# Performance work log

Hardware: AMD Instinct MI355X
Metric: run time of the kernel (lower is better)

The kernel has to match this reference:

```python
import math
import jax, jax.numpy as jnp
import numpy as np

B, D, H, W, K = 32, 256, 64, 64, 6
CTX = 256
TEMP = 0.5
EPS_LN = 1e-5


def _layernorm(x, g, b):
    mu = x.mean(-1, keepdims=True)
    var = ((x - mu) ** 2).mean(-1, keepdims=True)
    return (x - mu) * jax.lax.rsqrt(var + EPS_LN) * g + b


def _linear(x, w, b):
    return x @ w.T + b


def _gru_cell(x, h, wih, bih, whh, bhh):
    gi = x @ wih.T + bih
    gh = h @ whh.T + bhh
    i_r, i_z, i_n = jnp.split(gi, 3, axis=-1)
    h_r, h_z, h_n = jnp.split(gh, 3, axis=-1)
    r = jax.nn.sigmoid(i_r + h_r)
    z = jax.nn.sigmoid(i_z + h_z)
    n = jnp.tanh(i_n + r * h_n)
    return (1.0 - z) * n + z * h


def setup_inputs() -> dict:
    key = jax.random.key(0)
    ks = jax.random.split(key, 24)
    s = 0.05
    p = {
        'features': jax.random.normal(ks[0], (B, D, H, W), jnp.float32),
        'task_context': jax.random.normal(ks[1], (B, CTX), jnp.float32),
        'ctx_w1': jax.random.normal(ks[2], (D, CTX), jnp.float32) * s,
        'ctx_b1': jnp.zeros((D,), jnp.float32),
        'ctx_w2': jax.random.normal(ks[3], (K * D, D), jnp.float32) * s,
        'ctx_b2': jnp.zeros((K * D,), jnp.float32),
        'q_w': jax.random.normal(ks[4], (D, D), jnp.float32) * s,
        'q_b': jnp.zeros((D,), jnp.float32),
        'k_w': jax.random.normal(ks[5], (D, D), jnp.float32) * s,
        'k_b': jnp.zeros((D,), jnp.float32),
        'v_w': jax.random.normal(ks[6], (D, D), jnp.float32) * s,
        'v_b': jnp.zeros((D,), jnp.float32),
        'qn_g': jnp.ones((D,), jnp.float32),
        'qn_b': jnp.zeros((D,), jnp.float32),
        'fn_g': jnp.ones((D,), jnp.float32),
        'fn_b': jnp.zeros((D,), jnp.float32),
        'stop_w1': jax.random.normal(ks[7], (D // 2, D + 1), jnp.float32) * s,
        'stop_b1': jnp.zeros((D // 2,), jnp.float32),
        'stop_w2': jax.random.normal(ks[8], (1, D // 2), jnp.float32) * s,
        'stop_b2': jnp.zeros((1,), jnp.float32),
        'gru_wih': jax.random.normal(ks[9], (3 * D, D), jnp.float32) * s,
        'gru_bih': jnp.zeros((3 * D,), jnp.float32),
        'gru_whh': jax.random.normal(ks[10], (3 * D, D), jnp.float32) * s,
        'gru_bhh': jnp.zeros((3 * D,), jnp.float32),
    }
    return p


def _forward(features, task_context, ctx_w1, ctx_b1, ctx_w2, ctx_b2,
             q_w, q_b, k_w, k_b, v_w, v_b, qn_g, qn_b, fn_g, fn_b,
             stop_w1, stop_b1, stop_w2, stop_b2,
             gru_wih, gru_bih, gru_whh, gru_bhh):
    scale = math.sqrt(D)
    N = H * W
    # task-conditioned clue queries: (B, K, D), clamped
    h1 = jax.nn.gelu(_linear(task_context, ctx_w1, ctx_b1), approximate=False)
    clue_queries = _linear(h1, ctx_w2, ctx_b2).reshape(B, K, D)
    clue_queries = jnp.clip(clue_queries, -10.0, 10.0)

    # (B, N, D), normalized; k/v projections are loop-invariant -> hoist
    feats = jnp.transpose(features, (0, 2, 3, 1)).reshape(B, N, D)
    feats = _layernorm(feats, fn_g, fn_b)
    kp = _linear(feats, k_w, k_b)  # (B, N, D)
    vp = _linear(feats, v_w, v_b)  # (B, N, D)

    rows = jnp.repeat(jnp.arange(H, dtype=jnp.float32), W)  # (N,)
    cols = jnp.tile(jnp.arange(W, dtype=jnp.float32), H)    # (N,)
    max_entropy = math.log(N + 1e-6)

    def step(carry, qk):
        query_state, cum_mask = carry  # (B,D), (B,N)
        query = _layernorm(qk + query_state, qn_g, qn_b)
        q = _linear(query, q_w, q_b)  # (B, D)
        scores = jnp.einsum('bd,bnd->bn', q, kp) / scale
        scores = scores + jnp.log(jnp.clip(cum_mask, 1e-6))
        scores = jnp.clip(scores, -50.0, 50.0)
        logits = jnp.clip(scores / max(TEMP, 1e-10), -50.0, 50.0)
        attn = jnp.clip(jax.nn.softmax(logits, axis=-1), 1e-8)  # (B, N)
        row_c = attn @ rows
        col_c = attn @ cols
        centroid = jnp.stack([row_c, col_c], axis=-1)  # (B, 2)
        attended = jnp.einsum('bn,bnd->bd', attn, vp)  # (B, D)
        new_state = _gru_cell(attended, query_state, gru_wih, gru_bih, gru_whh, gru_bhh)
        a = jnp.clip(attn, 1e-6)
        entropy = -(a * jnp.log(a)).sum(-1, keepdims=True) / max_entropy
        s1 = jax.nn.gelu(_linear(jnp.concatenate([attended, entropy], -1), stop_w1, stop_b1), approximate=False)
        stop_raw = _linear(s1, stop_w2, stop_b2)[:, 0]
        stop = 4.0 * jnp.tanh(stop_raw / 4.0)
        new_mask = jnp.clip(cum_mask * (1.0 - 0.9 * jax.lax.stop_gradient(attn)), 1e-6)
        return (new_state, new_mask), (centroid, attn.reshape(B, H, W), stop)

    init = (jnp.zeros((B, D), jnp.float32), jnp.ones((B, N), jnp.float32))
    qks = jnp.transpose(clue_queries, (1, 0, 2))  # (K, B, D)
    _, (cents, attns, stops) = jax.lax.scan(step, init, qks)
    centroids = jnp.transpose(cents, (1, 0, 2))        # (B, K, 2)
    attention_maps = jnp.transpose(attns, (1, 0, 2, 3))  # (B, K, H, W)
    stop_logits = jnp.transpose(stops, (1, 0))          # (B, K)
    return centroids, attention_maps, stop_logits


def reference(features, task_context, ctx_w1, ctx_b1, ctx_w2, ctx_b2,
              q_w, q_b, k_w, k_b, v_w, v_b, qn_g, qn_b, fn_g, fn_b,
              stop_w1, stop_b1, stop_w2, stop_b2,
              gru_wih, gru_bih, gru_whh, gru_bhh):
    return _forward(features, task_context, ctx_w1, ctx_b1, ctx_w2, ctx_b2,
                    q_w, q_b, k_w, k_b, v_w, v_b, qn_g, qn_b, fn_g, fn_b,
                    stop_w1, stop_b1, stop_w2, stop_b2,
                    gru_wih, gru_bih, gru_whh, gru_bhh)
```

## Files before the change

### kernel.cpp

```cpp
#include <hip/hip_runtime.h>
#include <hip/hip_bf16.h>

#define NB 32
#define ND 256
#define NN_ 4096
#define NK 6

typedef short bf16x8 __attribute__((ext_vector_type(8)));
typedef float f32x4 __attribute__((ext_vector_type(4)));

__device__ __forceinline__ float bf2f(unsigned int u) {
    union { unsigned int i; float f; } v; v.i = (u & 0xffffu) << 16; return v.f;
}
__device__ __forceinline__ unsigned short f2bf(float f) {
    __hip_bfloat16 h = __float2bfloat16(f);
    return *reinterpret_cast<unsigned short*>(&h);
}
__device__ __forceinline__ float gelu_exact(float x) {
    return 0.5f * x * (1.0f + erff(x * 0.70710678118654752f));
}

__global__ void k_setup(const float* __restrict__ kw, const float* __restrict__ vw,
                        unsigned short* __restrict__ kwb, unsigned short* __restrict__ vwb,
                        float* __restrict__ mask, float* __restrict__ accs,
                        float* __restrict__ sumev0,
                        const float* __restrict__ tc, const float* __restrict__ w1,
                        const float* __restrict__ b1, const float* __restrict__ w2,
                        const float* __restrict__ b2, float* __restrict__ clue) {
    __shared__ __align__(16) float tcs[256];
    __shared__ __align__(16) float h1[256];
    int blk = blockIdx.x, t = threadIdx.x;
    if (blk < 1059) {
        int i = blk * 256 + t;
        if (i < 65536) kwb[i] = f2bf(kw[i]);
        else if (i < 131072) vwb[i - 65536] = f2bf(vw[i - 65536]);
        else if (i < 262144) mask[i - 131072] = 1.f;
        else if (i < 262912) accs[i - 262144] = 0.f;
        else if (i < 271104) sumev0[i - 262912] = 0.f;
        return;
    }
    int b = blk - 1059;
    tcs[t] = tc[b * 256 + t];
    __syncthreads();
    const float4* wr = (const float4*)(w1 + (size_t)t * 256);
    const float4* xs = (const float4*)tcs;
    float acc = b1[t];
#pragma unroll 8
    for (int i = 0; i < 64; ++i) {
        float4 w = wr[i], x = xs[i];
        acc += w.x * x.x + w.y * x.y + w.z * x.z + w.w * x.w;
    }
    h1[t] = gelu_exact(acc);
    __syncthreads();
    const float4* hs = (const float4*)h1;
    for (int r = 0; r < 6; ++r) {
        int row = r * 256 + t;
        const float4* w2r = (const float4*)(w2 + (size_t)row * 256);
        float a2 = b2[row];
#pragma unroll 8
        for (int i = 0; i < 64; ++i) {
            float4 w = w2r[i], x = hs[i];
            a2 += w.x * x.x + w.y * x.y + w.z * x.z + w.w * x.w;
        }
        clue[b * 1536 + row] = fminf(fmaxf(a2, -10.f), 10.f);
    }
}

__global__ __launch_bounds__(256, 2) void k_kv(
    const float* __restrict__ features, const float* __restrict__ fn_g,
    const float* __restrict__ fn_b, const unsigned short* __restrict__ kwb,
    const unsigned short* __restrict__ vwb, const float* __restrict__ kb,
    const float* __restrict__ vb, unsigned short* __restrict__ kp,
    unsigned short* __restrict__ vp) {
    int tile = blockIdx.x, b = blockIdx.y;
    int n0 = tile * 128;
    int t = threadIdx.x;

    __shared__ __align__(16) unsigned short A[32768];
    unsigned int* A32 = reinterpret_cast<unsigned int*>(A);

    int dd = t & 15, nq = t >> 4;
#pragma unroll
    for (int hh = 0; hh < 2; ++hh) {
        const float* fb = features + (size_t)b * 1048576 + n0 + hh * 64 + nq * 4;
        unsigned int pk[8][4];
        float s[4] = {0, 0, 0, 0}, s2[4] = {0, 0, 0, 0};
#pragma unroll
        for (int p = 0; p < 8; ++p) {
            int d0 = p * 32 + dd * 2;
            float4 a0 = *reinterpret_cast<const float4*>(fb + (size_t)d0 * 4096);
            float4 a1 = *reinterpret_cast<const float4*>(fb + (size_t)(d0 + 1) * 4096);
            s[0] += a0.x + a1.x; s2[0] += a0.x * a0.x + a1.x * a1.x;
            s[1] += a0.y + a1.y; s2[1] += a0.y * a0.y + a1.y * a1.y;
            s[2] += a0.z + a1.z; s2[2] += a0.z * a0.z + a1.z * a1.z;
            s[3] += a0.w + a1.w; s2[3] += a0.w * a0.w + a1.w * a1.w;
            pk[p][0] = (unsigned int)f2bf(a0.x) | ((unsigned int)f2bf(a1.x) << 16);
            pk[p][1] = (unsigned int)f2bf(a0.y) | ((unsigned int)f2bf(a1.y) << 16);
            pk[p][2] = (unsigned int)f2bf(a0.z) | ((unsigned int)f2bf(a1.z) << 16);
            pk[p][3] = (unsigned int)f2bf(a0.w) | ((unsigned int)f2bf(a1.w) << 16);
        }
#pragma unroll
        for (int m = 1; m < 16; m <<= 1) {
#pragma unroll
            for (int k = 0; k < 4; ++k) {
                s[k] += __shfl_xor(s[k], m, 64);
                s2[k] += __shfl_xor(s2[k], m, 64);
            }
        }
        float mm[4], rr[4];
#pragma unroll
        for (int k = 0; k < 4; ++k) {
            float mean = s[k] * (1.f / 256.f);
            float var = s2[k] * (1.f / 256.f) - mean * mean;
            mm[k] = mean; rr[k] = rsqrtf(var + 1e-5f);
        }
        int qdw = dd >> 2, jw = dd & 3;
#pragma unroll
        for (int p = 0; p < 8; ++p) {
            int d0 = p * 32 + dd * 2;
            float g0 = fn_g[d0], g1 = fn_g[d0 + 1];
            float e0 = fn_b[d0], e1 = fn_b[d0 + 1];
#pragma unroll
            for (int k = 0; k < 4; ++k) {
                int ln = hh * 64 + nq * 4 + k;
                int nt = ln >> 4, r = ln & 15;
                float x0 = bf2f(pk[p][k]);
                float x1 = bf2f(pk[p][k] >> 16);
                unsigned int lo = f2bf((x0 - mm[k]) * rr[k] * g0 + e0);
                unsigned int hi = f2bf((x1 - mm[k]) * rr[k] * g1 + e1);
                A32[((nt * 8 + p) * 64 + qdw * 16 + r) * 4 + jw] = lo | (hi << 16);
            }
        }
    }
    __syncthreads();

    int lane = t & 63, wv = t >> 6;
    int r = lane & 15, qd = lane >> 4;
#pragma unroll
    for (int ntt = 0; ntt < 2; ++ntt) {
        bf16x8 bfrag[4][8];
#pragma unroll
        for (int q4 = 0; q4 < 4; ++q4)
#pragma unroll
            for (int ks = 0; ks < 8; ++ks)
                bfrag[q4][ks] = *reinterpret_cast<const bf16x8*>(
                    &A[(((ntt * 4 + q4) * 8 + ks) * 64 + lane) * 8]);
#pragma unroll
        for (int mat = 0; mat < 2; ++mat) {
            const unsigned short* wb = mat ? vwb : kwb;
            const float* bias = mat ? vb : kb;
            unsigned short* outp = mat ? vp : kp;
#pragma unroll
            for (int dtl = 0; dtl < 4; ++dtl) {
                int dt = wv * 4 + dtl;
                const unsigned short* wrow = wb + (size_t)(dt * 16 + r) * 256 + qd * 8;
                f32x4 acc0 = {0, 0, 0, 0}, acc1 = {0, 0, 0, 0};
                f32x4 acc2 = {0, 0, 0, 0}, acc3 = {0, 0, 0, 0};
#pragma unroll
                for (int ks = 0; ks < 8; ++ks) {
                    bf16x8 af = *reinterpret_cast<const bf16x8*>(wrow + ks * 32);
                    acc0 = __builtin_amdgcn_mfma_f32_16x16x32_bf16(af, bfrag[0][ks], acc0, 0, 0, 0);
                    acc1 = __builtin_amdgcn_mfma_f32_16x16x32_bf16(af, bfrag[1][ks], acc1, 0, 0, 0);
                    acc2 = __builtin_amdgcn_mfma_f32_16x16x32_bf16(af, bfrag[2][ks], acc2, 0, 0, 0);
                    acc3 = __builtin_amdgcn_mfma_f32_16x16x32_bf16(af, bfrag[3][ks], acc3, 0, 0, 0);
                }
                int dbase = dt * 16 + qd * 4;
                float b0_ = bias[dbase], b1_ = bias[dbase + 1];
                float b2_ = bias[dbase + 2], b3_ = bias[dbase + 3];
                f32x4 aa[4] = {acc0, acc1, acc2, acc3};
#pragma unroll
                for (int q4 = 0; q4 < 4; ++q4) {
                    int n_g = n0 + (ntt * 4 + q4) * 16 + r;
                    unsigned int lo = ((unsigned int)f2bf(aa[q4][1] + b1_) << 16)
                                    | (unsigned int)f2bf(aa[q4][0] + b0_);
                    unsigned int hi = ((unsigned int)f2bf(aa[q4][3] + b3_) << 16)
                                    | (unsigned int)f2bf(aa[q4][2] + b2_);
                    *reinterpret_cast<uint2*>(outp + ((size_t)(b * 4096 + n_g)) * 256 + dbase)
                        = make_uint2(lo, hi);
                }
            }
        }
    }
}

__global__ __launch_bounds__(256, 4) void k_qscore(
    const float* __restrict__ clue, const float* __restrict__ gacc,
    const float* __restrict__ state_prev, float* __restrict__ state_cur,
    const float* __restrict__ qn_g, const float* __restrict__ qn_b,
    const float* __restrict__ q_w, const float* __restrict__ q_b,
    const unsigned short* __restrict__ kp, const unsigned short* __restrict__ vp,
    const float* __restrict__ mask, float* __restrict__ escore,
    float* __restrict__ accs, float* __restrict__ sumev,
    const float* __restrict__ sumev_prev,
    const float* __restrict__ sw1, const float* __restrict__ sb1,
    const float* __restrict__ sw2, const float* __restrict__ sb2,
    float* __restrict__ out_cent, float* __restrict__ out_stop, int kstep) {
    int c = blockIdx.x, b = blockIdx.y, t = threadIdx.x;
    int lane = t & 63, wv = t >> 6;
    __shared__ __align__(16) float qs[256];
    __shared__ float ash[256];
    __shared__ __align__(16) float part[8][264];
    __shared__ float sred[8];
    if (c == 16) {
        if (kstep == 0) return;
        int kp_ = kstep - 1;
        float inv = 1.f / accs[kp_ * 128 + b];
        qs[t] = sumev_prev[b * 256 + t] * inv;
        __syncthreads();
        float entv = -accs[kp_ * 128 + 96 + b] * 0.12022458674074826f;
        float v = 0.f;
        if (t < 128) {
            const float* wr = sw1 + (size_t)t * 257;
            float acc = sb1[t];
#pragma unroll 8
            for (int i = 0; i < 256; ++i) acc += qs[i] * wr[i];
            acc += entv * wr[256];
            v = gelu_exact(acc) * sw2[t];
        }
#pragma unroll
        for (int off = 32; off > 0; off >>= 1) v += __shfl_down(v, off, 64);
        if (lane == 0) sred[wv] = v;
        __syncthreads();
        if (t == 0) {
            float sraw = sb2[0] + sred[0] + sred[1] + sred[2] + sred[3];
            out_stop[b * 6 + kp_] = 4.f * tanhf(sraw * 0.25f);
            out_cent[(b * 6 + kp_) * 2 + 0] = accs[kp_ * 128 + 32 + b];
            out_cent[(b * 6 + kp_) * 2 + 1] = accs[kp_ * 128 + 64 + b];
        }
        return;
    }
    float h = 0.f;
    if (kstep > 0) {
        float sr = gacc[(b * 4 + 0) * 256 + t];
        float sz = gacc[(b * 4 + 1) * 256 + t];
        float gin = gacc[(b * 4 + 2) * 256 + t];
        float ghn = gacc[(b * 4 + 3) * 256 + t];
        float r = 1.f / (1.f + expf(-sr));
        float z = 1.f / (1.f + expf(-sz));
        float nv = tanhf(gin + r * ghn);
        h = (1.f - z) * nv + z * state_prev[b * 256 + t];
    }
    if (c == 0) state_cur[b * 256 + t] = h;
    float x = clue[(b * 6 + kstep) * 256 + t] + h;
    float s = x, s2 = x * x;
#pragma unroll
    for (int off = 32; off > 0; off >>= 1) {
        s += __shfl_down(s, off, 64);
        s2 += __shfl_down(s2, off, 64);
    }
    if (lane == 0) { sred[wv] = s; sred[4 + wv] = s2; }
    __syncthreads();
    float muv = (sred[0] + sred[1] + sred[2] + sred[3]) * (1.f / 256.f);
    float var = (sred[4] + sred[5] + sred[6] + sred[7]) * (1.f / 256.f) - muv * muv;
    float rs = rsqrtf(var + 1e-5f);
    qs[t] = (x - muv) * rs * qn_g[t] + qn_b[t];
    __syncthreads();
    const float4* wr = (const float4*)(q_w + (size_t)t * 256);
    const float4* xs4 = (const float4*)qs;
    float qv = q_b[t];
#pragma unroll 8
    for (int i = 0; i < 64; ++i) {
        float4 w = wr[i], xx = xs4[i];
        qv += w.x * xx.x + w.y * xx.y + w.z * xx.z + w.w * xx.w;
    }
    __syncthreads();
    qs[t] = qv;
    __syncthreads();
    int l = t & 7, rg = t >> 3;
    float dsum = 0.f;
#pragma unroll
    for (int pp = 0; pp < 8; ++pp) {
        int nl = pp * 32 + rg;
        int n = c * 256 + nl;
        const uint4* kr = reinterpret_cast<const uint4*>(kp + ((size_t)(b * 4096 + n)) * 256 + l * 8);
        float dot = 0.f;
#pragma unroll
        for (int j = 0; j < 4; ++j) {
            uint4 rv = kr[j * 8];
            const float* qq = qs + j * 64 + l * 8;
            dot += bf2f(rv.x) * qq[0] + bf2f(rv.x >> 16) * qq[1]
                 + bf2f(rv.y) * qq[2] + bf2f(rv.y >> 16) * qq[3]
                 + bf2f(rv.z) * qq[4] + bf2f(rv.z >> 16) * qq[5]
                 + bf2f(rv.w) * qq[6] + bf2f(rv.w >> 16) * qq[7];
        }
        dot += __shfl_xor(dot, 1, 64);
        dot += __shfl_xor(dot, 2, 64);
        dot += __shfl_xor(dot, 4, 64);
        float sc = dot * 0.0625f + logf(mask[(size_t)b * 4096 + n]);
        sc = fminf(fmaxf(sc, -50.f), 50.f);
        float lg = fminf(fmaxf(sc * 2.f, -50.f), 50.f);
        float e = expf(lg);
        if (l == 0) {
            escore[(size_t)b * 4096 + n] = e;
            ash[nl] = e;
        }
        dsum += e;
    }
    dsum *= 0.125f;
#pragma unroll
    for (int off = 32; off > 0; off >>= 1) dsum += __shfl_down(dsum, off, 64);
    if (lane == 0) sred[wv] = dsum;
    __syncthreads();
    if (t == 0) atomicAdd(&accs[kstep * 128 + b], sred[0] + sred[1] + sred[2] + sred[3]);
    int dbase = (t & 31) * 8, noff = t >> 5;
    const unsigned short* vb = vp + ((size_t)(b * 4096 + c * 256 + noff * 32)) * 256 + dbase;
    float a0 = 0, a1 = 0, a2 = 0, a3 = 0, a4 = 0, a5 = 0, a6 = 0, a7 = 0;
#pragma unroll 4
    for (int j = 0; j < 32; ++j) {
        uint4 rv = *reinterpret_cast<const uint4*>(vb + (size_t)j * 256);
        float w = ash[noff * 32 + j];
        a0 += w * bf2f(rv.x); a1 += w * bf2f(rv.x >> 16);
        a2 += w * bf2f(rv.y); a3 += w * bf2f(rv.y >> 16);
        a4 += w * bf2f(rv.z); a5 += w * bf2f(rv.z >> 16);
        a6 += w * bf2f(rv.w); a7 += w * bf2f(rv.w >> 16);
    }
    *reinterpret_cast<float4*>(&part[noff][dbase])     = make_float4(a0, a1, a2, a3);
    *reinterpret_cast<float4*>(&part[noff][dbase + 4]) = make_float4(a4, a5, a6, a7);
    __syncthreads();
    float sum = part[0][t] + part[1][t] + part[2][t] + part[3][t]
              + part[4][t] + part[5][t] + part[6][t] + part[7][t];
    atomicAdd(&sumev[b * 256 + t], sum);
}

__global__ __launch_bounds__(256, 2) void k_attn2gate(
    const float* __restrict__ escore, float* __restrict__ mask,
    float* __restrict__ accs, float* __restrict__ out_amap,
    const float* __restrict__ sumev, float* __restrict__ sumev_zero,
    const float* __restrict__ state_cur,
    const float* __restrict__ wih, const float* __restrict__ bih,
    const float* __restrict__ whh, const float* __restrict__ bhh,
    float* __restrict__ gacc, int kstep) {
    int bb = blockIdx.x, t = threadIdx.x;
    int lane = t & 63, wv = t >> 6;
    __shared__ __align__(16) float att[256];
    __shared__ __align__(16) float st[256];
    __shared__ float sred[12];
    if (bb < 128) {
        int b = bb & 31, c = bb >> 5;
        int n4 = (c * 256 + t) * 4;
        float inv = 1.f / accs[kstep * 128 + b];
        float4 e4 = *reinterpret_cast<const float4*>(&escore[(size_t)b * 4096 + n4]);
        float4 m4 = *reinterpret_cast<const float4*>(&mask[(size_t)b * 4096 + n4]);
        float a[4] = {fmaxf(e4.x * inv, 1e-8f), fmaxf(e4.y * inv, 1e-8f),
                      fmaxf(e4.z * inv, 1e-8f), fmaxf(e4.w * inv, 1e-8f)};
        *reinterpret_cast<float4*>(&out_amap[((size_t)(b * 6 + kstep)) * 4096 + n4])
            = make_float4(a[0], a[1], a[2], a[3]);
        float mv[4] = {m4.x, m4.y, m4.z, m4.w};
        float s0 = 0.f, s1 = 0.f, s2 = 0.f;
#pragma unroll
        for (int j = 0; j < 4; ++j) {
            int n = n4 + j;
            s0 += a[j] * (float)(n >> 6);
            s1 += a[j] * (float)(n & 63);
            float ac = fmaxf(a[j], 1e-6f);
            s2 += ac * logf(ac);
            mv[j] = fmaxf(mv[j] * (1.f - 0.9f * a[j]), 1e-6f);
        }
        *reinterpret_cast<float4*>(&mask[(size_t)b * 4096 + n4])
            = make_float4(mv[0], mv[1], mv[2], mv[3]);
#pragma unroll
        for (int off = 32; off > 0; off >>= 1) {
            s0 += __shfl_down(s0, off, 64);
            s1 += __shfl_down(s1, off, 64);
            s2 += __shfl_down(s2, off, 64);
        }
        if (lane == 0) { sred[wv] = s0; sred[4 + wv] = s1; sred[8 + wv] = s2; }
        __syncthreads();
        if (t == 0) {
            atomicAdd(&accs[kstep * 128 + 32 + b], sred[0] + sred[1] + sred[2] + sred[3]);
            atomicAdd(&accs[kstep * 128 + 64 + b], sred[4] + sred[5] + sred[6] + sred[7]);
            atomicAdd(&accs[kstep * 128 + 96 + b], sred[8] + sred[9] + sred[10] + sred[11]);
        }
    } else if (bb < 224) {
        if (kstep == 5) return;
        int b = (bb - 128) & 31, g = (bb - 128) >> 5;
        float inv = 1.f / accs[kstep * 128 + b];
        att[t] = sumev[b * 256 + t] * inv;
        st[t] = state_cur[b * 256 + t];
        __syncthreads();
        int row = g * 256 + t;
        const float4* wi = (const float4*)(wih + (size_t)row * 256);
        const float4* wh = (const float4*)(whh + (size_t)row * 256);
        const float4* av = (const float4*)att;
        const float4* sv = (const float4*)st;
        float ai = bih[row], ah = bhh[row];
#pragma unroll 4
        for (int i = 0; i < 64; ++i) {
            float4 w1 = wi[i], x1 = av[i];
            ai += w1.x * x1.x + w1.y * x1.y + w1.z * x1.z + w1.w * x1.w;
            float4 w2 = wh[i], x2 = sv[i];
            ah += w2.x * x2.x + w2.y * x2.y + w2.z * x2.z + w2.w * x2.w;
        }
        if (g == 2) {
            gacc[(b * 4 + 2) * 256 + t] = ai;
            gacc[(b * 4 + 3) * 256 + t] = ah;
        } else {
            gacc[(b * 4 + g) * 256 + t] = ai + ah;
        }
    } else {
        int b = bb - 224;
        sumev_zero[b * 256 + t] = 0.f;
    }
}

__global__ void k_stop5(const float* __restrict__ sumev, const float* __restrict__ accs,
                        const float* __restrict__ sw1, const float* __restrict__ sb1,
                        const float* __restrict__ sw2, const float* __restrict__ sb2,
                        float* __restrict__ out_cent, float* __restrict__ out_stop) {
    int b = blockIdx.x, t = threadIdx.x;
    int lane = t & 63, wv = t >> 6;
    __shared__ __align__(16) float att[256];
    __shared__ float sred[4];
    float inv = 1.f / accs[5 * 128 + b];
    att[t] = sumev[b * 256 + t] * inv;
    __syncthreads();
    float entv = -accs[5 * 128 + 96 + b] * 0.12022458674074826f;
    float v = 0.f;
    if (t < 128) {
        const float* wr = sw1 + (size_t)t * 257;
        float acc = sb1[t];
#pragma unroll 8
        for (int i = 0; i < 256; ++i) acc += att[i] * wr[i];
        acc += entv * wr[256];
        v = gelu_exact(acc) * sw2[t];
    }
#pragma unroll
    for (int off = 32; off > 0; off >>= 1) v += __shfl_down(v, off, 64);
    if (lane == 0) sred[wv] = v;
    __syncthreads();
    if (t == 0) {
        float sraw = sb2[0] + sred[0] + sred[1] + sred[2] + sred[3];
        out_stop[b * 6 + 5] = 4.f * tanhf(sraw * 0.25f);
        out_cent[(b * 6 + 5) * 2 + 0] = accs[5 * 128 + 32 + b];
        out_cent[(b * 6 + 5) * 2 + 1] = accs[5 * 128 + 64 + b];
    }
}

extern "C" void kernel_launch(void* const* d_in, const int* in_sizes, int n_in,
                              void* d_out, int out_size, void* d_ws, size_t ws_size,
                              hipStream_t stream) {
    const float* features     = (const float*)d_in[0];
    const float* task_context = (const float*)d_in[1];
    const float* ctx_w1 = (const float*)d_in[2];
    const float* ctx_b1 = (const float*)d_in[3];
    const float* ctx_w2 = (const float*)d_in[4];
    const float* ctx_b2 = (const float*)d_in[5];
    const float* q_w = (const float*)d_in[6];
    const float* q_b = (const float*)d_in[7];
    const float* k_w = (const float*)d_in[8];
    const float* k_b = (const float*)d_in[9];
    const float* v_w = (const float*)d_in[10];
    const float* v_b = (const float*)d_in[11];
    const float* qn_g = (const float*)d_in[12];
    const float* qn_b = (const float*)d_in[13];
    const float* fn_g = (const float*)d_in[14];
    const float* fn_b = (const float*)d_in[15];
    const float* stop_w1 = (const float*)d_in[16];
    const float* stop_b1 = (const float*)d_in[17];
    const float* stop_w2 = (const float*)d_in[18];
    const float* stop_b2 = (const float*)d_in[19];
    const float* gru_wih = (const float*)d_in[20];
    const float* gru_bih = (const float*)d_in[21];
    const float* gru_whh = (const float*)d_in[22];
    const float* gru_bhh = (const float*)d_in[23];

    unsigned short* kwb = (unsigned short*)d_ws;
    unsigned short* vwb = kwb + 65536;
    unsigned short* kp  = vwb + 65536;
    unsigned short* vp  = kp + (size_t)NB * NN_ * ND;
    float* clue     = (float*)(vp + (size_t)NB * NN_ * ND);
    float* state0   = clue + NB * NK * ND;
    float* state1   = state0 + NB * ND;
    float* sumev0   = state1 + NB * ND;
    float* sumev1   = sumev0 + NB * ND;
    float* mask     = sumev1 + NB * ND;
    float* escore   = mask + NB * NN_;
    float* accs     = escore + NB * NN_;
    float* gacc     = accs + NK * 4 * NB;

    float* out_cent = (float*)d_out;
    float* out_amap = out_cent + NB * NK * 2;
    float* out_stop = out_amap + (size_t)NB * NK * NN_;

    float* stbuf[2] = {state0, state1};
    float* evbuf[2] = {sumev0, sumev1};

    k_setup<<<1091, 256, 0, stream>>>(k_w, v_w, kwb, vwb, mask, accs, sumev0,
                                      task_context, ctx_w1, ctx_b1, ctx_w2, ctx_b2, clue);
    k_kv<<<dim3(32, 32), 256, 0, stream>>>(features, fn_g, fn_b, kwb, vwb, k_b, v_b, kp, vp);
    for (int k = 0; k < NK; ++k) {
        float* scur = stbuf[k & 1];
        float* sprev = stbuf[1 - (k & 1)];
        float* ev = evbuf[k & 1];
        float* evo = evbuf[1 - (k & 1)];
        k_qscore<<<dim3(17, 32), 256, 0, stream>>>(clue, gacc, sprev, scur, qn_g, qn_b,
                                                   q_w, q_b, kp, vp, mask, escore, accs,
                                                   ev, evo, stop_w1, stop_b1, stop_w2, stop_b2,
                                                   out_cent, out_stop, k);
        k_attn2gate<<<256, 256, 0, stream>>>(escore, mask, accs, out_amap, ev, evo, scur,
                                             gru_wih, gru_bih, gru_whh, gru_bhh, gacc, k);
    }
    k_stop5<<<32, 256, 0, stream>>>(evbuf[1], accs, stop_w1, stop_b1, stop_w2, stop_b2,
                                    out_cent, out_stop);
}
```

Before: 733.5 us.

## Fuse GRU and query projection into attn kernel; retile K/V layout and scoring

Moves the GRU update, LayerNorm and query projection out of every scoring block into the per-batch gate kernel, and seeds the first query in setup. This removes work that was redundantly recomputed across all score blocks. K/V are now stored in a d-tile-major layout and built with 64-row tiles at higher occupancy. The score grid is doubled. The weighted-V accumulation now writes per-block partial buffers that are summed later instead of using atomics, which also removes the zeroing pass but adds extra reads of the partials.

```diff
diff --git a/kernel.cpp b/kernel.cpp
--- a/kernel.cpp
+++ b/kernel.cpp
@@ -23,12 +23,16 @@
 __global__ void k_setup(const float* __restrict__ kw, const float* __restrict__ vw,
                         unsigned short* __restrict__ kwb, unsigned short* __restrict__ vwb,
                         float* __restrict__ mask, float* __restrict__ accs,
-                        float* __restrict__ sumev0,
+                        float* __restrict__ state,
                         const float* __restrict__ tc, const float* __restrict__ w1,
                         const float* __restrict__ b1, const float* __restrict__ w2,
-                        const float* __restrict__ b2, float* __restrict__ clue) {
+                        const float* __restrict__ b2, float* __restrict__ clue,
+                        const float* __restrict__ qn_g, const float* __restrict__ qn_b,
+                        const float* __restrict__ q_w, const float* __restrict__ q_b,
+                        float* __restrict__ qbuf) {
     __shared__ __align__(16) float tcs[256];
     __shared__ __align__(16) float h1[256];
+    __shared__ float sred[8];
     int blk = blockIdx.x, t = threadIdx.x;
     if (blk < 1059) {
         int i = blk * 256 + t;
@@ -36,23 +40,26 @@
         else if (i < 131072) vwb[i - 65536] = f2bf(vw[i - 65536]);
         else if (i < 262144) mask[i - 131072] = 1.f;
         else if (i < 262912) accs[i - 262144] = 0.f;
-        else if (i < 271104) sumev0[i - 262912] = 0.f;
+        else state[i - 262912] = 0.f;
         return;
     }
     int b = blk - 1059;
+    int lane = t & 63, wv = t >> 6;
     tcs[t] = tc[b * 256 + t];
     __syncthreads();
-    const float4* wr = (const float4*)(w1 + (size_t)t * 256);
-    const float4* xs = (const float4*)tcs;
+    const float4* wr1 = (const float4*)(w1 + (size_t)t * 256);
+    const float4* xs1 = (const float4*)tcs;
     float acc = b1[t];
 #pragma unroll 8
     for (int i = 0; i < 64; ++i) {
-        float4 w = wr[i], x = xs[i];
+        float4 w = wr1[i], x = xs1[i];
         acc += w.x * x.x + w.y * x.y + w.z * x.z + w.w * x.w;
     }
+    __syncthreads();
     h1[t] = gelu_exact(acc);
     __syncthreads();
     const float4* hs = (const float4*)h1;
+    float x0 = 0.f;
     for (int r = 0; r < 6; ++r) {
         int row = r * 256 + t;
         const float4* w2r = (const float4*)(w2 + (size_t)row * 256);
@@ -62,74 +69,95 @@
             float4 w = w2r[i], x = hs[i];
             a2 += w.x * x.x + w.y * x.y + w.z * x.z + w.w * x.w;
         }
-        clue[b * 1536 + row] = fminf(fmaxf(a2, -10.f), 10.f);
-    }
-}
-
-__global__ __launch_bounds__(256, 2) void k_kv(
+        float cv = fminf(fmaxf(a2, -10.f), 10.f);
+        clue[b * 1536 + row] = cv;
+        if (r == 0) x0 = cv;
+    }
+    float s = x0, s2 = x0 * x0;
+#pragma unroll
+    for (int off = 32; off > 0; off >>= 1) {
+        s += __shfl_down(s, off, 64);
+        s2 += __shfl_down(s2, off, 64);
+    }
+    if (lane == 0) { sred[wv] = s; sred[4 + wv] = s2; }
+    __syncthreads();
+    float mu = (sred[0] + sred[1] + sred[2] + sred[3]) * (1.f / 256.f);
+    float var = (sred[4] + sred[5] + sred[6] + sred[7]) * (1.f / 256.f) - mu * mu;
+    float rs = rsqrtf(var + 1e-5f);
+    tcs[t] = (x0 - mu) * rs * qn_g[t] + qn_b[t];
+    __syncthreads();
+    const float4* wr = (const float4*)(q_w + (size_t)t * 256);
+    const float4* xs = (const float4*)tcs;
+    float qv = q_b[t];
+#pragma unroll 8
+    for (int i = 0; i < 64; ++i) {
+        float4 w = wr[i], xx = xs[i];
+        qv += w.x * xx.x + w.y * xx.y + w.z * xx.z + w.w * xx.w;
+    }
+    qbuf[b * 256 + t] = qv;
+}
+
+__global__ __launch_bounds__(256, 4) void k_kv(
     const float* __restrict__ features, const float* __restrict__ fn_g,
     const float* __restrict__ fn_b, const unsigned short* __restrict__ kwb,
     const unsigned short* __restrict__ vwb, const float* __restrict__ kb,
     const float* __restrict__ vb, unsigned short* __restrict__ kp,
     unsigned short* __restrict__ vp) {
     int tile = blockIdx.x, b = blockIdx.y;
-    int n0 = tile * 128;
+    int n0 = tile * 64;
     int t = threadIdx.x;
 
-    __shared__ __align__(16) unsigned short A[32768];
+    __shared__ __align__(16) unsigned short A[16384];
     unsigned int* A32 = reinterpret_cast<unsigned int*>(A);
 
     int dd = t & 15, nq = t >> 4;
-#pragma unroll
-    for (int hh = 0; hh < 2; ++hh) {
-        const float* fb = features + (size_t)b * 1048576 + n0 + hh * 64 + nq * 4;
-        unsigned int pk[8][4];
-        float s[4] = {0, 0, 0, 0}, s2[4] = {0, 0, 0, 0};
-#pragma unroll
-        for (int p = 0; p < 8; ++p) {
-            int d0 = p * 32 + dd * 2;
-            float4 a0 = *reinterpret_cast<const float4*>(fb + (size_t)d0 * 4096);
-            float4 a1 = *reinterpret_cast<const float4*>(fb + (size_t)(d0 + 1) * 4096);
-            s[0] += a0.x + a1.x; s2[0] += a0.x * a0.x + a1.x * a1.x;
-            s[1] += a0.y + a1.y; s2[1] += a0.y * a0.y + a1.y * a1.y;
-            s[2] += a0.z + a1.z; s2[2] += a0.z * a0.z + a1.z * a1.z;
-            s[3] += a0.w + a1.w; s2[3] += a0.w * a0.w + a1.w * a1.w;
-            pk[p][0] = (unsigned int)f2bf(a0.x) | ((unsigned int)f2bf(a1.x) << 16);
-            pk[p][1] = (unsigned int)f2bf(a0.y) | ((unsigned int)f2bf(a1.y) << 16);
-            pk[p][2] = (unsigned int)f2bf(a0.z) | ((unsigned int)f2bf(a1.z) << 16);
-            pk[p][3] = (unsigned int)f2bf(a0.w) | ((unsigned int)f2bf(a1.w) << 16);
-        }
-#pragma unroll
-        for (int m = 1; m < 16; m <<= 1) {
-#pragma unroll
-            for (int k = 0; k < 4; ++k) {
-                s[k] += __shfl_xor(s[k], m, 64);
-                s2[k] += __shfl_xor(s2[k], m, 64);
-            }
-        }
-        float mm[4], rr[4];
+    const float* fb = features + (size_t)b * 1048576 + n0 + nq * 4;
+    unsigned int pk[8][4];
+    float s[4] = {0, 0, 0, 0}, s2[4] = {0, 0, 0, 0};
+#pragma unroll
+    for (int p = 0; p < 8; ++p) {
+        int d0 = p * 32 + dd * 2;
+        float4 a0 = *reinterpret_cast<const float4*>(fb + (size_t)d0 * 4096);
+        float4 a1 = *reinterpret_cast<const float4*>(fb + (size_t)(d0 + 1) * 4096);
+        s[0] += a0.x + a1.x; s2[0] += a0.x * a0.x + a1.x * a1.x;
+        s[1] += a0.y + a1.y; s2[1] += a0.y * a0.y + a1.y * a1.y;
+        s[2] += a0.z + a1.z; s2[2] += a0.z * a0.z + a1.z * a1.z;
+        s[3] += a0.w + a1.w; s2[3] += a0.w * a0.w + a1.w * a1.w;
+        pk[p][0] = (unsigned int)f2bf(a0.x) | ((unsigned int)f2bf(a1.x) << 16);
+        pk[p][1] = (unsigned int)f2bf(a0.y) | ((unsigned int)f2bf(a1.y) << 16);
+        pk[p][2] = (unsigned int)f2bf(a0.z) | ((unsigned int)f2bf(a1.z) << 16);
+        pk[p][3] = (unsigned int)f2bf(a0.w) | ((unsigned int)f2bf(a1.w) << 16);
+    }
+#pragma unroll
+    for (int m = 1; m < 16; m <<= 1) {
 #pragma unroll
         for (int k = 0; k < 4; ++k) {
-            float mean = s[k] * (1.f / 256.f);
-            float var = s2[k] * (1.f / 256.f) - mean * mean;
-            mm[k] = mean; rr[k] = rsqrtf(var + 1e-5f);
-        }
-        int qdw = dd >> 2, jw = dd & 3;
-#pragma unroll
-        for (int p = 0; p < 8; ++p) {
-            int d0 = p * 32 + dd * 2;
-            float g0 = fn_g[d0], g1 = fn_g[d0 + 1];
-            float e0 = fn_b[d0], e1 = fn_b[d0 + 1];
-#pragma unroll
-            for (int k = 0; k < 4; ++k) {
-                int ln = hh * 64 + nq * 4 + k;
-                int nt = ln >> 4, r = ln & 15;
-                float x0 = bf2f(pk[p][k]);
-                float x1 = bf2f(pk[p][k] >> 16);
-                unsigned int lo = f2bf((x0 - mm[k]) * rr[k] * g0 + e0);
-                unsigned int hi = f2bf((x1 - mm[k]) * rr[k] * g1 + e1);
-                A32[((nt * 8 + p) * 64 + qdw * 16 + r) * 4 + jw] = lo | (hi << 16);
-            }
+            s[k] += __shfl_xor(s[k], m, 64);
+            s2[k] += __shfl_xor(s2[k], m, 64);
+        }
+    }
+    float mm[4], rr[4];
+#pragma unroll
+    for (int k = 0; k < 4; ++k) {
+        float mean = s[k] * (1.f / 256.f);
+        float var = s2[k] * (1.f / 256.f) - mean * mean;
+        mm[k] = mean; rr[k] = rsqrtf(var + 1e-5f);
+    }
+    int qdw = dd >> 2, jw = dd & 3;
+#pragma unroll
+    for (int p = 0; p < 8; ++p) {
+        int d0 = p * 32 + dd * 2;
+        float g0 = fn_g[d0], g1 = fn_g[d0 + 1];
+        float e0 = fn_b[d0], e1 = fn_b[d0 + 1];
+#pragma unroll
+        for (int k = 0; k < 4; ++k) {
+            int ln = nq * 4 + k;
+            int nt = ln >> 4, r = ln & 15;
+            float x0 = bf2f(pk[p][k]);
+            float x1 = bf2f(pk[p][k] >> 16);
+            unsigned int lo = f2bf((x0 - mm[k]) * rr[k] * g0 + e0);
+            unsigned int hi = f2bf((x1 - mm[k]) * rr[k] * g1 + e1);
+            A32[((nt * 8 + p) * 64 + qdw * 16 + r) * 4 + jw] = lo | (hi << 16);
         }
     }
     __syncthreads();
@@ -137,14 +165,14 @@
     int lane = t & 63, wv = t >> 6;
     int r = lane & 15, qd = lane >> 4;
 #pragma unroll
-    for (int ntt = 0; ntt < 2; ++ntt) {
-        bf16x8 bfrag[4][8];
-#pragma unroll
-        for (int q4 = 0; q4 < 4; ++q4)
+    for (int q2 = 0; q2 < 2; ++q2) {
+        bf16x8 bfrag[2][8];
+#pragma unroll
+        for (int q = 0; q < 2; ++q)
 #pragma unroll
             for (int ks = 0; ks < 8; ++ks)
-                bfrag[q4][ks] = *reinterpret_cast<const bf16x8*>(
-                    &A[(((ntt * 4 + q4) * 8 + ks) * 64 + lane) * 8]);
+                bfrag[q][ks] = *reinterpret_cast<const bf16x8*>(
+                    &A[(((q2 * 2 + q) * 8 + ks) * 64 + lane) * 8]);
 #pragma unroll
         for (int mat = 0; mat < 2; ++mat) {
             const unsigned short* wb = mat ? vwb : kwb;
@@ -155,27 +183,25 @@
                 int dt = wv * 4 + dtl;
                 const unsigned short* wrow = wb + (size_t)(dt * 16 + r) * 256 + qd * 8;
                 f32x4 acc0 = {0, 0, 0, 0}, acc1 = {0, 0, 0, 0};
-                f32x4 acc2 = {0, 0, 0, 0}, acc3 = {0, 0, 0, 0};
 #pragma unroll
                 for (int ks = 0; ks < 8; ++ks) {
                     bf16x8 af = *reinterpret_cast<const bf16x8*>(wrow + ks * 32);
                     acc0 = __builtin_amdgcn_mfma_f32_16x16x32_bf16(af, bfrag[0][ks], acc0, 0, 0, 0);
                     acc1 = __builtin_amdgcn_mfma_f32_16x16x32_bf16(af, bfrag[1][ks], acc1, 0, 0, 0);
-                    acc2 = __builtin_amdgcn_mfma_f32_16x16x32_bf16(af, bfrag[2][ks], acc2, 0, 0, 0);
-                    acc3 = __builtin_amdgcn_mfma_f32_16x16x32_bf16(af, bfrag[3][ks], acc3, 0, 0, 0);
                 }
                 int dbase = dt * 16 + qd * 4;
                 float b0_ = bias[dbase], b1_ = bias[dbase + 1];
                 float b2_ = bias[dbase + 2], b3_ = bias[dbase + 3];
-                f32x4 aa[4] = {acc0, acc1, acc2, acc3};
-#pragma unroll
-                for (int q4 = 0; q4 < 4; ++q4) {
-                    int n_g = n0 + (ntt * 4 + q4) * 16 + r;
-                    unsigned int lo = ((unsigned int)f2bf(aa[q4][1] + b1_) << 16)
-                                    | (unsigned int)f2bf(aa[q4][0] + b0_);
-                    unsigned int hi = ((unsigned int)f2bf(aa[q4][3] + b3_) << 16)
-                                    | (unsigned int)f2bf(aa[q4][2] + b2_);
-                    *reinterpret_cast<uint2*>(outp + ((size_t)(b * 4096 + n_g)) * 256 + dbase)
+                f32x4 aa[2] = {acc0, acc1};
+#pragma unroll
+                for (int q = 0; q < 2; ++q) {
+                    int n_g = n0 + (q2 * 2 + q) * 16 + r;
+                    unsigned int lo = ((unsigned int)f2bf(aa[q][1] + b1_) << 16)
+                                    | (unsigned int)f2bf(aa[q][0] + b0_);
+                    unsigned int hi = ((unsigned int)f2bf(aa[q][3] + b3_) << 16)
+                                    | (unsigned int)f2bf(aa[q][2] + b2_);
+                    *reinterpret_cast<uint2*>(
+                        outp + ((size_t)(b * 16 + dt) * 4096 + n_g) * 16 + qd * 4)
                         = make_uint2(lo, hi);
                 }
             }
@@ -184,28 +210,27 @@
 }
 
 __global__ __launch_bounds__(256, 4) void k_qscore(
-    const float* __restrict__ clue, const float* __restrict__ gacc,
-    const float* __restrict__ state_prev, float* __restrict__ state_cur,
-    const float* __restrict__ qn_g, const float* __restrict__ qn_b,
-    const float* __restrict__ q_w, const float* __restrict__ q_b,
-    const unsigned short* __restrict__ kp, const unsigned short* __restrict__ vp,
-    const float* __restrict__ mask, float* __restrict__ escore,
-    float* __restrict__ accs, float* __restrict__ sumev,
-    const float* __restrict__ sumev_prev,
+    const float* __restrict__ qbuf, const unsigned short* __restrict__ kp,
+    const unsigned short* __restrict__ vp, const float* __restrict__ mask,
+    float* __restrict__ escore, float* __restrict__ accs,
+    float* __restrict__ pb_cur, const float* __restrict__ pb_prev,
     const float* __restrict__ sw1, const float* __restrict__ sb1,
     const float* __restrict__ sw2, const float* __restrict__ sb2,
     float* __restrict__ out_cent, float* __restrict__ out_stop, int kstep) {
     int c = blockIdx.x, b = blockIdx.y, t = threadIdx.x;
     int lane = t & 63, wv = t >> 6;
     __shared__ __align__(16) float qs[256];
-    __shared__ float ash[256];
+    __shared__ float ash[128];
     __shared__ __align__(16) float part[8][264];
     __shared__ float sred[8];
-    if (c == 16) {
+    if (c == 32) {
         if (kstep == 0) return;
         int kp_ = kstep - 1;
         float inv = 1.f / accs[kp_ * 128 + b];
-        qs[t] = sumev_prev[b * 256 + t] * inv;
+        float a = 0.f;
+#pragma unroll
+        for (int c2 = 0; c2 < 32; ++c2) a += pb_prev[((size_t)c2 * 32 + b) * 256 + t];
+        qs[t] = a * inv;
         __syncthreads();
         float entv = -accs[kp_ * 128 + 96 + b] * 0.12022458674074826f;
         float v = 0.f;
@@ -229,60 +254,36 @@
         }
         return;
     }
-    float h = 0.f;
-    if (kstep > 0) {
-        float sr = gacc[(b * 4 + 0) * 256 + t];
-        float sz = gacc[(b * 4 + 1) * 256 + t];
-        float gin = gacc[(b * 4 + 2) * 256 + t];
-        float ghn = gacc[(b * 4 + 3) * 256 + t];
-        float r = 1.f / (1.f + expf(-sr));
-        float z = 1.f / (1.f + expf(-sz));
-        float nv = tanhf(gin + r * ghn);
-        h = (1.f - z) * nv + z * state_prev[b * 256 + t];
-    }
-    if (c == 0) state_cur[b * 256 + t] = h;
-    float x = clue[(b * 6 + kstep) * 256 + t] + h;
-    float s = x, s2 = x * x;
-#pragma unroll
-    for (int off = 32; off > 0; off >>= 1) {
-        s += __shfl_down(s, off, 64);
-        s2 += __shfl_down(s2, off, 64);
-    }
-    if (lane == 0) { sred[wv] = s; sred[4 + wv] = s2; }
-    __syncthreads();
-    float muv = (sred[0] + sred[1] + sred[2] + sred[3]) * (1.f / 256.f);
-    float var = (sred[4] + sred[5] + sred[6] + sred[7]) * (1.f / 256.f) - muv * muv;
-    float rs = rsqrtf(var + 1e-5f);
-    qs[t] = (x - muv) * rs * qn_g[t] + qn_b[t];
-    __syncthreads();
-    const float4* wr = (const float4*)(q_w + (size_t)t * 256);
-    const float4* xs4 = (const float4*)qs;
-    float qv = q_b[t];
-#pragma unroll 8
-    for (int i = 0; i < 64; ++i) {
-        float4 w = wr[i], xx = xs4[i];
-        qv += w.x * xx.x + w.y * xx.y + w.z * xx.z + w.w * xx.w;
-    }
-    __syncthreads();
-    qs[t] = qv;
+    qs[t] = qbuf[b * 256 + t];
     __syncthreads();
     int l = t & 7, rg = t >> 3;
+    const float* qq = qs + l * 32;
     float dsum = 0.f;
 #pragma unroll
-    for (int pp = 0; pp < 8; ++pp) {
+    for (int pp = 0; pp < 4; ++pp) {
         int nl = pp * 32 + rg;
-        int n = c * 256 + nl;
-        const uint4* kr = reinterpret_cast<const uint4*>(kp + ((size_t)(b * 4096 + n)) * 256 + l * 8);
-        float dot = 0.f;
-#pragma unroll
-        for (int j = 0; j < 4; ++j) {
-            uint4 rv = kr[j * 8];
-            const float* qq = qs + j * 64 + l * 8;
-            dot += bf2f(rv.x) * qq[0] + bf2f(rv.x >> 16) * qq[1]
-                 + bf2f(rv.y) * qq[2] + bf2f(rv.y >> 16) * qq[3]
-                 + bf2f(rv.z) * qq[4] + bf2f(rv.z >> 16) * qq[5]
-                 + bf2f(rv.w) * qq[6] + bf2f(rv.w >> 16) * qq[7];
-        }
+        int n = c * 128 + nl;
+        const uint4* base = reinterpret_cast<const uint4*>(
+            kp + ((size_t)(b * 16 + l * 2) * 4096 + n) * 16);
+        uint4 r0 = base[0], r1 = base[1];
+        uint4 r2 = base[8192], r3 = base[8193];
+        float dot =
+              bf2f(r0.x) * qq[0]  + bf2f(r0.x >> 16) * qq[1]
+            + bf2f(r0.y) * qq[2]  + bf2f(r0.y >> 16) * qq[3]
+            + bf2f(r0.z) * qq[4]  + bf2f(r0.z >> 16) * qq[5]
+            + bf2f(r0.w) * qq[6]  + bf2f(r0.w >> 16) * qq[7]
+            + bf2f(r1.x) * qq[8]  + bf2f(r1.x >> 16) * qq[9]
+            + bf2f(r1.y) * qq[10] + bf2f(r1.y >> 16) * qq[11]
+            + bf2f(r1.z) * qq[12] + bf2f(r1.z >> 16) * qq[13]
+            + bf2f(r1.w) * qq[14] + bf2f(r1.w >> 16) * qq[15]
+            + bf2f(r2.x) * qq[16] + bf2f(r2.x >> 16) * qq[17]
+            + bf2f(r2.y) * qq[18] + bf2f(r2.y >> 16) * qq[19]
+            + bf2f(r2.z) * qq[20] + bf2f(r2.z >> 16) * qq[21]
+            + bf2f(r2.w) * qq[22] + bf2f(r2.w >> 16) * qq[23]
+            + bf2f(r3.x) * qq[24] + bf2f(r3.x >> 16) * qq[25]
+            + bf2f(r3.y) * qq[26] + bf2f(r3.y >> 16) * qq[27]
+            + bf2f(r3.z) * qq[28] + bf2f(r3.z >> 16) * qq[29]
+            + bf2f(r3.w) * qq[30] + bf2f(r3.w >> 16) * qq[31];
         dot += __shfl_xor(dot, 1, 64);
         dot += __shfl_xor(dot, 2, 64);
         dot += __shfl_xor(dot, 4, 64);
@@ -302,34 +303,38 @@
     if (lane == 0) sred[wv] = dsum;
     __syncthreads();
     if (t == 0) atomicAdd(&accs[kstep * 128 + b], sred[0] + sred[1] + sred[2] + sred[3]);
-    int dbase = (t & 31) * 8, noff = t >> 5;
-    const unsigned short* vb = vp + ((size_t)(b * 4096 + c * 256 + noff * 32)) * 256 + dbase;
+    int ds_ = t & 31, noff = t >> 5;
+    int dt = ds_ >> 1, qh = (ds_ & 1) * 8;
+    const unsigned short* vb = vp + ((size_t)(b * 16 + dt) * 4096 + c * 128 + noff * 16) * 16 + qh;
     float a0 = 0, a1 = 0, a2 = 0, a3 = 0, a4 = 0, a5 = 0, a6 = 0, a7 = 0;
 #pragma unroll 4
-    for (int j = 0; j < 32; ++j) {
-        uint4 rv = *reinterpret_cast<const uint4*>(vb + (size_t)j * 256);
-        float w = ash[noff * 32 + j];
+    for (int j = 0; j < 16; ++j) {
+        uint4 rv = *reinterpret_cast<const uint4*>(vb + (size_t)j * 16);
+        float w = ash[noff * 16 + j];
         a0 += w * bf2f(rv.x); a1 += w * bf2f(rv.x >> 16);
         a2 += w * bf2f(rv.y); a3 += w * bf2f(rv.y >> 16);
         a4 += w * bf2f(rv.z); a5 += w * bf2f(rv.z >> 16);
         a6 += w * bf2f(rv.w); a7 += w * bf2f(rv.w >> 16);
     }
+    int dbase = ds_ * 8;
     *reinterpret_cast<float4*>(&part[noff][dbase])     = make_float4(a0, a1, a2, a3);
     *reinterpret_cast<float4*>(&part[noff][dbase + 4]) = make_float4(a4, a5, a6, a7);
     __syncthreads();
     float sum = part[0][t] + part[1][t] + part[2][t] + part[3][t]
               + part[4][t] + part[5][t] + part[6][t] + part[7][t];
-    atomicAdd(&sumev[b * 256 + t], sum);
+    pb_cur[((size_t)c * 32 + b) * 256 + t] = sum;
 }
 
 __global__ __launch_bounds__(256, 2) void k_attn2gate(
     const float* __restrict__ escore, float* __restrict__ mask,
     float* __restrict__ accs, float* __restrict__ out_amap,
-    const float* __restrict__ sumev, float* __restrict__ sumev_zero,
-    const float* __restrict__ state_cur,
+    const float* __restrict__ pbuf, float* __restrict__ state,
+    const float* __restrict__ clue,
+    const float* __restrict__ qn_g, const float* __restrict__ qn_b,
+    const float* __restrict__ q_w, const float* __restrict__ q_b,
     const float* __restrict__ wih, const float* __restrict__ bih,
     const float* __restrict__ whh, const float* __restrict__ bhh,
-    float* __restrict__ gacc, int kstep) {
+    float* __restrict__ qbuf, int kstep) {
     int bb = blockIdx.x, t = threadIdx.x;
     int lane = t & 63, wv = t >> 6;
     __shared__ __align__(16) float att[256];
@@ -371,18 +376,26 @@
             atomicAdd(&accs[kstep * 128 + 64 + b], sred[4] + sred[5] + sred[6] + sred[7]);
             atomicAdd(&accs[kstep * 128 + 96 + b], sred[8] + sred[9] + sred[10] + sred[11]);
         }
-    } else if (bb < 224) {
-        if (kstep == 5) return;
-        int b = (bb - 128) & 31, g = (bb - 128) >> 5;
-        float inv = 1.f / accs[kstep * 128 + b];
-        att[t] = sumev[b * 256 + t] * inv;
-        st[t] = state_cur[b * 256 + t];
-        __syncthreads();
+        return;
+    }
+    if (kstep == 5) return;
+    int b = bb - 128;
+    float inv = 1.f / accs[kstep * 128 + b];
+    float a = 0.f;
+#pragma unroll
+    for (int c2 = 0; c2 < 32; ++c2) a += pbuf[((size_t)c2 * 32 + b) * 256 + t];
+    float hprev = state[b * 256 + t];
+    att[t] = a * inv;
+    st[t] = hprev;
+    __syncthreads();
+    const float4* av = (const float4*)att;
+    const float4* sv = (const float4*)st;
+    float gsum[3], hsum[3];
+#pragma unroll
+    for (int g = 0; g < 3; ++g) {
         int row = g * 256 + t;
         const float4* wi = (const float4*)(wih + (size_t)row * 256);
         const float4* wh = (const float4*)(whh + (size_t)row * 256);
-        const float4* av = (const float4*)att;
-        const float4* sv = (const float4*)st;
         float ai = bih[row], ah = bhh[row];
 #pragma unroll 4
         for (int i = 0; i < 64; ++i) {
@@ -391,19 +404,39 @@
             float4 w2 = wh[i], x2 = sv[i];
             ah += w2.x * x2.x + w2.y * x2.y + w2.z * x2.z + w2.w * x2.w;
         }
-        if (g == 2) {
-            gacc[(b * 4 + 2) * 256 + t] = ai;
-            gacc[(b * 4 + 3) * 256 + t] = ah;
-        } else {
-            gacc[(b * 4 + g) * 256 + t] = ai + ah;
-        }
-    } else {
-        int b = bb - 224;
-        sumev_zero[b * 256 + t] = 0.f;
-    }
-}
-
-__global__ void k_stop5(const float* __restrict__ sumev, const float* __restrict__ accs,
+        gsum[g] = ai; hsum[g] = ah;
+    }
+    float rg_ = 1.f / (1.f + expf(-(gsum[0] + hsum[0])));
+    float zg  = 1.f / (1.f + expf(-(gsum[1] + hsum[1])));
+    float ng  = tanhf(gsum[2] + rg_ * hsum[2]);
+    float h = (1.f - zg) * ng + zg * hprev;
+    state[b * 256 + t] = h;
+    float x = clue[((size_t)b * 6 + kstep + 1) * 256 + t] + h;
+    float s = x, s2 = x * x;
+#pragma unroll
+    for (int off = 32; off > 0; off >>= 1) {
+        s += __shfl_down(s, off, 64);
+        s2 += __shfl_down(s2, off, 64);
+    }
+    if (lane == 0) { sred[wv] = s; sred[4 + wv] = s2; }
+    __syncthreads();
+    float mu = (sred[0] + sred[1] + sred[2] + sred[3]) * (1.f / 256.f);
+    float var = (sred[4] + sred[5] + sred[6] + sred[7]) * (1.f / 256.f) - mu * mu;
+    float rs = rsqrtf(var + 1e-5f);
+    att[t] = (x - mu) * rs * qn_g[t] + qn_b[t];
+    __syncthreads();
+    const float4* wr = (const float4*)(q_w + (size_t)t * 256);
+    const float4* xs = (const float4*)att;
+    float qv = q_b[t];
+#pragma unroll 8
+    for (int i = 0; i < 64; ++i) {
+        float4 w = wr[i], xx = xs[i];
+        qv += w.x * xx.x + w.y * xx.y + w.z * xx.z + w.w * xx.w;
+    }
+    qbuf[b * 256 + t] = qv;
+}
+
+__global__ void k_stop5(const float* __restrict__ pbuf, const float* __restrict__ accs,
                         const float* __restrict__ sw1, const float* __restrict__ sb1,
                         const float* __restrict__ sw2, const float* __restrict__ sb2,
                         float* __restrict__ out_cent, float* __restrict__ out_stop) {
@@ -412,7 +445,10 @@
     __shared__ __align__(16) float att[256];
     __shared__ float sred[4];
     float inv = 1.f / accs[5 * 128 + b];
-    att[t] = sumev[b * 256 + t] * inv;
+    float a = 0.f;
+#pragma unroll
+    for (int c2 = 0; c2 < 32; ++c2) a += pbuf[((size_t)c2 * 32 + b) * 256 + t];
+    att[t] = a * inv;
     __syncthreads();
     float entv = -accs[5 * 128 + 96 + b] * 0.12022458674074826f;
     float v = 0.f;
@@ -468,38 +504,34 @@
     unsigned short* vwb = kwb + 65536;
     unsigned short* kp  = vwb + 65536;
     unsigned short* vp  = kp + (size_t)NB * NN_ * ND;
-    float* clue     = (float*)(vp + (size_t)NB * NN_ * ND);
-    float* state0   = clue + NB * NK * ND;
-    float* state1   = state0 + NB * ND;
-    float* sumev0   = state1 + NB * ND;
-    float* sumev1   = sumev0 + NB * ND;
-    float* mask     = sumev1 + NB * ND;
-    float* escore   = mask + NB * NN_;
-    float* accs     = escore + NB * NN_;
-    float* gacc     = accs + NK * 4 * NB;
+    float* clue   = (float*)(vp + (size_t)NB * NN_ * ND);
+    float* state  = clue + NB * NK * ND;
+    float* qbuf   = state + NB * ND;
+    float* mask   = qbuf + NB * ND;
+    float* escore = mask + NB * NN_;
+    float* accs   = escore + NB * NN_;
+    float* pbuf0  = accs + NK * 4 * NB;
+    float* pbuf1  = pbuf0 + 32 * NB * ND;
 
     float* out_cent = (float*)d_out;
     float* out_amap = out_cent + NB * NK * 2;
     float* out_stop = out_amap + (size_t)NB * NK * NN_;
 
-    float* stbuf[2] = {state0, state1};
-    float* evbuf[2] = {sumev0, sumev1};
-
-    k_setup<<<1091, 256, 0, stream>>>(k_w, v_w, kwb, vwb, mask, accs, sumev0,
-                                      task_context, ctx_w1, ctx_b1, ctx_w2, ctx_b2, clue);
-    k_kv<<<dim3(32, 32), 256, 0, stream>>>(features, fn_g, fn_b, kwb, vwb, k_b, v_b, kp, vp);
+    float* pb[2] = {pbuf0, pbuf1};
+
+    k_setup<<<1091, 256, 0, stream>>>(k_w, v_w, kwb, vwb, mask, accs, state,
+                                      task_context, ctx_w1, ctx_b1, ctx_w2, ctx_b2, clue,
+                                      qn_g, qn_b, q_w, q_b, qbuf);
+    k_kv<<<dim3(64, 32), 256, 0, stream>>>(features, fn_g, fn_b, kwb, vwb, k_b, v_b, kp, vp);
     for (int k = 0; k < NK; ++k) {
-        float* scur = stbuf[k & 1];
-        float* sprev = stbuf[1 - (k & 1)];
-        float* ev = evbuf[k & 1];
-        float* evo = evbuf[1 - (k & 1)];
-        k_qscore<<<dim3(17, 32), 256, 0, stream>>>(clue, gacc, sprev, scur, qn_g, qn_b,
-                                                   q_w, q_b, kp, vp, mask, escore, accs,
-                                                   ev, evo, stop_w1, stop_b1, stop_w2, stop_b2,
+        k_qscore<<<dim3(33, 32), 256, 0, stream>>>(qbuf, kp, vp, mask, escore, accs,
+                                                   pb[k & 1], pb[(k + 1) & 1],
+                                                   stop_w1, stop_b1, stop_w2, stop_b2,
                                                    out_cent, out_stop, k);
-        k_attn2gate<<<256, 256, 0, stream>>>(escore, mask, accs, out_amap, ev, evo, scur,
-                                             gru_wih, gru_bih, gru_whh, gru_bhh, gacc, k);
-    }
-    k_stop5<<<32, 256, 0, stream>>>(evbuf[1], accs, stop_w1, stop_b1, stop_w2, stop_b2,
+        k_attn2gate<<<160, 256, 0, stream>>>(escore, mask, accs, out_amap, pb[k & 1], state,
+                                             clue, qn_g, qn_b, q_w, q_b,
+                                             gru_wih, gru_bih, gru_whh, gru_bhh, qbuf, k);
+    }
+    k_stop5<<<32, 256, 0, stream>>>(pb[1], accs, stop_w1, stop_b1, stop_w2, stop_b2,
                                     out_cent, out_stop);
 }
```

Measured after the change: 955.5 us. +30.3%, slower.
